# Performance work log

Hardware: AMD Instinct MI355X
Metric: run time of the kernel (lower is better)

Reference implementation:

```python
import jax, jax.numpy as jnp
import numpy as np

B, T, D_HID, D_TRK, N_TRANS = 128, 40, 512, 256, 64


def setup_inputs() -> dict:
    key = jax.random.key(0)
    ks = jax.random.split(key, 8)
    d, t = D_HID, D_TRK
    s = 0.05
    return {
        "buffers": jax.random.normal(ks[0], (B, T, 2 * d), jnp.float32),
        "W_left": jax.random.normal(ks[1], (5 * d, d), jnp.float32) * s,
        "b_left": jnp.zeros((5 * d,), jnp.float32),
        "W_right": jax.random.normal(ks[2], (5 * d, d), jnp.float32) * s,
        "W_track": jax.random.normal(ks[3], (5 * d, t), jnp.float32) * s,
        "W_ih": jax.random.normal(ks[4], (4 * t, 3 * d), jnp.float32) * s,
        "W_hh": jax.random.normal(ks[5], (4 * t, t), jnp.float32) * s,
        "b_ih": jnp.zeros((4 * t,), jnp.float32),
        "b_hh": jnp.zeros((4 * t,), jnp.float32),
        "W_trans": jax.random.normal(ks[6], (4, t), jnp.float32) * s,
        "b_trans": jnp.zeros((4,), jnp.float32),
        "transitions": jax.random.randint(ks[7], (N_TRANS, B), 0, 4),
    }


def _spinn_forward(buffers, W_left, b_left, W_right, W_track,
                   W_ih, W_hh, b_ih, b_hh, W_trans, b_trans, n_steps):
    # Thin-stack style vectorized SPINN: fixed-capacity stack + pointers.
    Bb, Tt, two_d = buffers.shape
    d = two_d // 2
    t = W_hh.shape[1]
    cap = Tt + 2  # stack never exceeds 2 initial + (T-2) shifts
    dtype = buffers.dtype

    stack0 = jnp.zeros((Bb, cap, two_d), dtype)
    # stacks = [buf[0], buf[0]] in the torch code
    stack0 = stack0.at[:, 0].set(buffers[:, 0]).at[:, 1].set(buffers[:, 0])
    sptr0 = jnp.full((Bb,), 2, jnp.int32)   # stack length
    blen0 = jnp.full((Bb,), Tt, jnp.int32)  # buffer length (pops from the end)
    th0 = jnp.zeros((Bb, t), dtype)
    tc0 = jnp.zeros((Bb, t), dtype)
    bidx = jnp.arange(Bb)

    def step(carry, _):
        stack, sptr, blen, th, tc = carry
        buf_top = buffers[bidx, blen - 1]          # buf[-1], [B, 2d]
        s1 = stack[bidx, sptr - 1]                 # stack[-1]
        s2 = stack[bidx, sptr - 2]                 # stack[-2]
        # Tracker LSTMCell on cat(buf_h, stack1_h, stack2_h)
        x = jnp.concatenate([buf_top[:, :d], s1[:, :d], s2[:, :d]], axis=1)
        gates = x @ W_ih.T + b_ih + th @ W_hh.T + b_hh
        gi, gf, gg, go = jnp.split(gates, 4, axis=1)
        tc_new = jax.nn.sigmoid(gf) * tc + jax.nn.sigmoid(gi) * jnp.tanh(gg)
        th_new = jax.nn.sigmoid(go) * jnp.tanh(tc_new)
        logits = th_new @ W_trans.T + b_trans      # [B, 4]
        trans = jnp.argmax(logits, axis=1)
        do_shift = (trans == 3) & (blen > 2)
        do_red = (trans == 2) & (sptr > 3)
        # REDUCE (TreeLSTM) computed for all rows, masked in below.
        # left = stack[-2], right = stack[-1] (right popped first in torch).
        lstm_in = (s2[:, :d] @ W_left.T + b_left
                   + s1[:, :d] @ W_right.T
                   + th_new @ W_track.T)           # [B, 5d]
        a, i_, f1, f2, o_ = jnp.split(lstm_in, 5, axis=1)
        c = (jnp.tanh(a) * jax.nn.sigmoid(i_)
             + jax.nn.sigmoid(f1) * s2[:, d:]
             + jax.nn.sigmoid(f2) * s1[:, d:])
        h = jax.nn.sigmoid(o_) * jnp.tanh(c)
        node = jnp.concatenate([h, c], axis=1)
        # SHIFT: push buf_top; REDUCE: overwrite stack[-2] and shrink by 1.
        stack = stack.at[bidx, sptr].set(
            jnp.where(do_shift[:, None], buf_top, stack[bidx, sptr]))
        stack = stack.at[bidx, sptr - 2].set(
            jnp.where(do_red[:, None], node, stack[bidx, sptr - 2]))
        sptr = sptr + do_shift.astype(jnp.int32) - do_red.astype(jnp.int32)
        blen = blen - do_shift.astype(jnp.int32)
        return (stack, sptr, blen, th_new, tc_new), logits

    _, all_logits = jax.lax.scan(step, (stack0, sptr0, blen0, th0, tc0),
                                 None, length=n_steps)
    return all_logits  # [n_steps, B, 4] = stacked trans_preds_batch


def reference(buffers, W_left, b_left, W_right, W_track, W_ih, W_hh,
              b_ih, b_hh, W_trans, b_trans, transitions):
    n_steps = transitions.shape[0]  # torch only uses transitions.size(0)
    return _spinn_forward(buffers, W_left, b_left, W_right, W_track,
                          W_ih, W_hh, b_ih, b_hh, W_trans, b_trans, n_steps)
```

## Files before the change

kernel.cpp:

```cpp
#include <hip/hip_runtime.h>
#include <math.h>


#define B_ 128
#define CAP 42
#define XW 2048
#define GSPLIT 14
#define LSPLIT 8

__device__ __forceinline__ float sigm(float x) { return 1.f / (1.f + expf(-x)); }

__global__ void k_repack(const float* __restrict__ W_ih, const float* __restrict__ W_hh,
                         const float* __restrict__ W_left, const float* __restrict__ W_right,
                         const float* __restrict__ W_track, const float* __restrict__ b_ih,
                         const float* __restrict__ b_hh,
                         float* __restrict__ W1T, float* __restrict__ W2T,
                         float* __restrict__ W3T, float* __restrict__ b1) {
    size_t idx = (size_t)blockIdx.x * 256 + threadIdx.x;
    const size_t n1 = 1792ull * 1024ull;
    const size_t n2 = 1024ull * 2560ull;
    const size_t n3 = 256ull * 2560ull;
    if (idx < n1) {
        int k = (int)(idx >> 10), n = (int)(idx & 1023);
        W1T[idx] = (k < 1536) ? W_ih[(size_t)n * 1536 + k] : W_hh[(size_t)n * 256 + (k - 1536)];
    } else if (idx < n1 + n2) {
        size_t r = idx - n1;
        int k = (int)(r / 2560), n = (int)(r % 2560);
        W2T[r] = (k < 512) ? W_right[(size_t)n * 512 + k] : W_left[(size_t)n * 512 + (k - 512)];
    } else if (idx < n1 + n2 + n3) {
        size_t r = idx - n1 - n2;
        int k = (int)(r / 2560), n = (int)(r % 2560);
        W3T[r] = W_track[(size_t)n * 256 + k];
    } else if (idx < n1 + n2 + n3 + 1024) {
        int i = (int)(idx - n1 - n2 - n3);
        b1[i] = b_ih[i] + b_hh[i];
    }
}

__global__ void k_init(const float* __restrict__ buffers, float* __restrict__ stack,
                       float* __restrict__ X, float* __restrict__ tc,
                       int* __restrict__ sptr, int* __restrict__ blen) {
    int b = blockIdx.x, t = threadIdx.x;
    const float* b0 = buffers + (size_t)b * 40 * 1024;
    const float* btop = b0 + 39 * 1024;
    float* stk = stack + (size_t)b * CAP * 1024;
    for (int j = t; j < 1024; j += 256) { stk[j] = b0[j]; stk[1024 + j] = b0[j]; }
    float* Xb = X + (size_t)b * XW;
    for (int j = t; j < 512; j += 256) {
        Xb[j] = btop[j]; Xb[512 + j] = b0[j]; Xb[1024 + j] = b0[j];
    }
    Xb[1536 + t] = 0.f;
    tc[b * 256 + t] = 0.f;
    if (t == 0) { sptr[b] = 2; blen[b] = 40; }
}

__global__ __launch_bounds__(256, 3) void k_gemm(const float* __restrict__ X,
                                                 const float* __restrict__ W1T,
                                                 const float* __restrict__ W2T,
                                                 float* __restrict__ gpart,
                                                 float* __restrict__ lpart) {
    __shared__ float As[32][132];
    __shared__ float Ws[32][68];
    const int bid = blockIdx.x;
    const float* WT; float* out; int N, n0, k0, aoff;
    if (bid < 224) {
        int ks = bid >> 4, nb = bid & 15;
        WT = W1T; out = gpart + (size_t)ks * 128 * 1024;
        N = 1024; n0 = nb * 64; k0 = ks * 128; aoff = 0;
    } else {
        int b2 = bid - 224; int ks = b2 / 40, nb = b2 % 40;
        WT = W2T; out = lpart + (size_t)ks * 128 * 2560;
        N = 2560; n0 = nb * 64; k0 = ks * 128; aoff = 512;
    }
    const int tid = threadIdx.x;
    const int tm = tid >> 4;
    const int tn = tid & 15;

    float acc[8][4];
#pragma unroll
    for (int i = 0; i < 8; i++)
#pragma unroll
        for (int j = 0; j < 4; j++) acc[i][j] = 0.f;

    for (int ki = 0; ki < 128; ki += 32) {
        const int kb = k0 + ki;
        __syncthreads();
        {
            int m = tid >> 1;
            int c8 = (tid & 1) * 16;
            const float4* src = (const float4*)(X + (size_t)m * XW + aoff + kb + c8);
#pragma unroll
            for (int j = 0; j < 4; j++) {
                float4 v = src[j];
                int kk = c8 + j * 4;
                As[kk + 0][m] = v.x; As[kk + 1][m] = v.y; As[kk + 2][m] = v.z; As[kk + 3][m] = v.w;
            }
        }
        {
            int kk = tid >> 3;
            int c = (tid & 7) * 8;
            const float4* src = (const float4*)(WT + (size_t)(kb + kk) * N + n0 + c);
            float4* dst = (float4*)(&Ws[kk][c]);
            dst[0] = src[0]; dst[1] = src[1];
        }
        __syncthreads();
#pragma unroll 4
        for (int kk = 0; kk < 32; kk++) {
            float a[8], w[4];
            *(float4*)&a[0] = *(const float4*)&As[kk][tm * 4];
            *(float4*)&a[4] = *(const float4*)&As[kk][64 + tm * 4];
            *(float4*)&w[0] = *(const float4*)&Ws[kk][tn * 4];
#pragma unroll
            for (int i = 0; i < 8; i++)
#pragma unroll
                for (int j = 0; j < 4; j++) acc[i][j] += a[i] * w[j];
        }
    }
    float* base = out + n0 + tn * 4;
#pragma unroll
    for (int i = 0; i < 8; i++) {
        int m = (i < 4) ? (tm * 4 + i) : (64 + tm * 4 + (i - 4));
        *(float4*)(base + (size_t)m * N) = make_float4(acc[i][0], acc[i][1], acc[i][2], acc[i][3]);
    }
}

__global__ __launch_bounds__(256) void k_B(const float* __restrict__ gpart,
                                           const float* __restrict__ lpart,
                                           const float* __restrict__ b1,
                                           const float* __restrict__ b_left,
                                           const float* __restrict__ W3T,
                                           const float* __restrict__ W_trans,
                                           const float* __restrict__ b_trans,
                                           const float* __restrict__ buffers,
                                           float* __restrict__ stack,
                                           float* __restrict__ X,
                                           const float* __restrict__ tc_in,
                                           float* __restrict__ tc_out,
                                           const int* __restrict__ sp_in,
                                           int* __restrict__ sp_out,
                                           const int* __restrict__ bl_in,
                                           int* __restrict__ bl_out,
                                           float* __restrict__ out_s) {
    const int bid = blockIdx.x;
    const int b = bid >> 2, q = bid & 3;
    const int t = threadIdx.x;
    const int sp = sp_in[b], bl = bl_in[b];

    const float* gp = gpart + (size_t)b * 1024;
    float gi = b1[t], gf = b1[256 + t], gg = b1[512 + t], go = b1[768 + t];
#pragma unroll
    for (int kc = 0; kc < GSPLIT; kc++) {
        const float* p = gp + (size_t)kc * 128 * 1024;
        gi += p[t]; gf += p[256 + t]; gg += p[512 + t]; go += p[768 + t];
    }
    float tcv = tc_in[b * 256 + t];
    float tcn = sigm(gf) * tcv + sigm(gi) * tanhf(gg);
    float thn = sigm(go) * tanhf(tcn);

    __shared__ float sh_th[256];
    __shared__ float red[256][4];
    sh_th[t] = thn;
    red[t][0] = thn * W_trans[t];
    red[t][1] = thn * W_trans[256 + t];
    red[t][2] = thn * W_trans[512 + t];
    red[t][3] = thn * W_trans[768 + t];
    __syncthreads();
    for (int off = 128; off > 0; off >>= 1) {
        if (t < off) {
            red[t][0] += red[t + off][0]; red[t][1] += red[t + off][1];
            red[t][2] += red[t + off][2]; red[t][3] += red[t + off][3];
        }
        __syncthreads();
    }
    float lg[4]; int tr = 0; float best = -1e30f;
#pragma unroll
    for (int l = 0; l < 4; l++) {
        lg[l] = red[0][l] + b_trans[l];
        if (lg[l] > best) { best = lg[l]; tr = l; }
    }
    if (q == 0 && t == 0) {
#pragma unroll
        for (int l = 0; l < 4; l++) out_s[b * 4 + l] = lg[l];
    }
    const bool do_shift = (tr == 3) && (bl > 2);
    const bool do_red   = (tr == 2) && (sp > 3);
    const int spn = sp + (do_shift ? 1 : 0) - (do_red ? 1 : 0);
    const int bln = bl - (do_shift ? 1 : 0);
    float* stk = stack + (size_t)b * CAP * 1024;

    float node_h = 0.f;
    if (do_red && t < 128) {
        const int j = q * 128 + t;
        const float* lp = lpart + (size_t)b * 2560;
        float a  = b_left[j],        ii = b_left[512 + j], f1 = b_left[1024 + j],
              f2 = b_left[1536 + j], oo = b_left[2048 + j];
#pragma unroll
        for (int kc = 0; kc < LSPLIT; kc++) {
            const float* p = lp + (size_t)kc * 128 * 2560;
            a += p[j]; ii += p[512 + j]; f1 += p[1024 + j]; f2 += p[1536 + j]; oo += p[2048 + j];
        }
        const float* w = W3T + j;
#pragma unroll 4
        for (int k = 0; k < 256; k++) {
            float th = sh_th[k];
            const float* wk = w + (size_t)k * 2560;
            a += th * wk[0]; ii += th * wk[512]; f1 += th * wk[1024];
            f2 += th * wk[1536]; oo += th * wk[2048];
        }
        float s1c = stk[(size_t)(sp - 1) * 1024 + 512 + j];
        float s2c = stk[(size_t)(sp - 2) * 1024 + 512 + j];
        float c = tanhf(a) * sigm(ii) + sigm(f1) * s2c + sigm(f2) * s1c;
        float h = sigm(oo) * tanhf(c);
        stk[(size_t)(sp - 2) * 1024 + j] = h;
        stk[(size_t)(sp - 2) * 1024 + 512 + j] = c;
        node_h = h;
    }
    if (do_shift) {
        const float* bt = buffers + ((size_t)b * 40 + (bl - 1)) * 1024;
        const int idx = q * 256 + t;
        stk[(size_t)sp * 1024 + idx] = bt[idx];
    }
    float* Xb = X + (size_t)b * XW;
    if (t < 128) {
        const int j = q * 128 + t;
        const float* btn = buffers + ((size_t)b * 40 + (bln - 1)) * 1024;
        Xb[j] = btn[j];
        float s1h;
        if (do_red)        s1h = node_h;
        else if (do_shift) s1h = buffers[((size_t)b * 40 + (bl - 1)) * 1024 + j];
        else               s1h = stk[(size_t)(sp - 1) * 1024 + j];
        Xb[512 + j] = s1h;
        Xb[1024 + j] = stk[(size_t)(spn - 2) * 1024 + j];
    }
    if ((t >> 6) == q) {
        Xb[1536 + t] = thn;
        tc_out[b * 256 + t] = tcn;
    }
    if (q == 0 && t == 0) { sp_out[b] = spn; bl_out[b] = bln; }
}

extern "C" void kernel_launch(void* const* d_in, const int* in_sizes, int n_in,
                              void* d_out, int out_size, void* d_ws, size_t ws_size,
                              hipStream_t stream) {
    const float* buffers = (const float*)d_in[0];
    const float* W_left  = (const float*)d_in[1];
    const float* b_left  = (const float*)d_in[2];
    const float* W_right = (const float*)d_in[3];
    const float* W_track = (const float*)d_in[4];
    const float* W_ih    = (const float*)d_in[5];
    const float* W_hh    = (const float*)d_in[6];
    const float* b_ih    = (const float*)d_in[7];
    const float* b_hh    = (const float*)d_in[8];
    const float* W_trans = (const float*)d_in[9];
    const float* b_trans = (const float*)d_in[10];
    float* out = (float*)d_out;

    float* ws = (float*)d_ws;
    size_t off = 0;
    float* W1T   = ws + off; off += 1792ull * 1024;
    float* W2T   = ws + off; off += 1024ull * 2560;
    float* W3T   = ws + off; off += 256ull * 2560;
    float* b1    = ws + off; off += 1024;
    float* X     = ws + off; off += (size_t)B_ * XW;
    float* tc_a  = ws + off; off += (size_t)B_ * 256;
    float* tc_b  = ws + off; off += (size_t)B_ * 256;
    float* gpart = ws + off; off += (size_t)GSPLIT * B_ * 1024;
    float* lpart = ws + off; off += (size_t)LSPLIT * B_ * 2560;
    float* stack = ws + off; off += (size_t)B_ * CAP * 1024;
    int* sp_a = (int*)(ws + off); off += 128;
    int* sp_b = (int*)(ws + off); off += 128;
    int* bl_a = (int*)(ws + off); off += 128;
    int* bl_b = (int*)(ws + off); off += 128;

    {
        size_t total = 1792ull * 1024 + 1024ull * 2560 + 256ull * 2560 + 1024;
        int blocks = (int)((total + 255) / 256);
        k_repack<<<blocks, 256, 0, stream>>>(W_ih, W_hh, W_left, W_right, W_track, b_ih, b_hh,
                                             W1T, W2T, W3T, b1);
        k_init<<<B_, 256, 0, stream>>>(buffers, stack, X, tc_a, sp_a, bl_a);
    }

    for (int s = 0; s < 64; s++) {
        k_gemm<<<544, 256, 0, stream>>>(X, W1T, W2T, gpart, lpart);
        const float* tci = (s & 1) ? tc_b : tc_a;  float* tco = (s & 1) ? tc_a : tc_b;
        const int*   spi = (s & 1) ? sp_b : sp_a;  int*   spo = (s & 1) ? sp_a : sp_b;
        const int*   bli = (s & 1) ? bl_b : bl_a;  int*   blo = (s & 1) ? bl_a : bl_b;
        k_B<<<512, 256, 0, stream>>>(gpart, lpart, b1, b_left, W3T, W_trans, b_trans,
                                     buffers, stack, X, tci, tco, spi, spo, bli, blo,
                                     out + (size_t)s * B_ * 4);
    }
    (void)in_sizes; (void)n_in; (void)out_size; (void)ws_size;
}
```

Baseline: 2.547 ms.

## Use 128x128 GEMM tiles with deeper split-K, wave-shuffle reduce, split W3T loop

Adds a GEMM mode that uses 128-wide output tiles with 8x8 per-thread accumulators and half the K-chunk per block, doubling the split-K partial count. Blocks therefore get higher arithmetic intensity while the grid stays at 544 blocks. The mode is chosen at runtime from workspace size, and k_B now sums a variable number of partials. k_B's logit reduction moves from a shared-memory tree to wavefront shuffles, and the reduce-path W3T dot product is split across both thread halves and combined through shared memory. Stack capacity and the X row width are trimmed. In exchange, k_B reads twice as many partial sums from memory and the GEMM kernel holds more registers per thread.

```diff
diff --git a/kernel.cpp b/kernel.cpp
--- a/kernel.cpp
+++ b/kernel.cpp
@@ -3,10 +3,9 @@
 
 
 #define B_ 128
-#define CAP 42
-#define XW 2048
-#define GSPLIT 14
-#define LSPLIT 8
+#define CAP 40
+#define XW 1792
+#define NSTEP 64
 
 __device__ __forceinline__ float sigm(float x) { return 1.f / (1.f + expf(-x)); }
 
@@ -58,69 +57,124 @@
                                                  const float* __restrict__ W1T,
                                                  const float* __restrict__ W2T,
                                                  float* __restrict__ gpart,
-                                                 float* __restrict__ lpart) {
+                                                 float* __restrict__ lpart, int mode) {
     __shared__ float As[32][132];
-    __shared__ float Ws[32][68];
+    __shared__ float Ws[32][132];
     const int bid = blockIdx.x;
-    const float* WT; float* out; int N, n0, k0, aoff;
-    if (bid < 224) {
-        int ks = bid >> 4, nb = bid & 15;
-        WT = W1T; out = gpart + (size_t)ks * 128 * 1024;
-        N = 1024; n0 = nb * 64; k0 = ks * 128; aoff = 0;
+    const int tid = threadIdx.x;
+    const int tm = tid >> 4, tn = tid & 15;
+
+    if (mode) {
+        const float* WT; float* out; int N, n0, k0, aoff;
+        if (bid < 224) {
+            int ks = bid >> 3, nb = bid & 7;
+            WT = W1T; out = gpart + (size_t)ks * 131072;
+            N = 1024; n0 = nb * 128; k0 = ks * 64; aoff = 0;
+        } else {
+            int tI = bid - 224; int ks = tI / 20, nb = tI % 20;
+            WT = W2T; out = lpart + (size_t)ks * 327680;
+            N = 2560; n0 = nb * 128; k0 = ks * 64; aoff = 512;
+        }
+        float acc[8][8];
+#pragma unroll
+        for (int i = 0; i < 8; i++)
+#pragma unroll
+            for (int j = 0; j < 8; j++) acc[i][j] = 0.f;
+
+        for (int ki = 0; ki < 64; ki += 32) {
+            const int kb = k0 + ki;
+            __syncthreads();
+            {
+                int m = tid >> 1, c8 = (tid & 1) * 16;
+                const float4* src = (const float4*)(X + (size_t)m * XW + aoff + kb + c8);
+#pragma unroll
+                for (int j = 0; j < 4; j++) {
+                    float4 v = src[j];
+                    int kk = c8 + j * 4;
+                    As[kk + 0][m] = v.x; As[kk + 1][m] = v.y; As[kk + 2][m] = v.z; As[kk + 3][m] = v.w;
+                }
+            }
+            {
+                int kk = tid >> 3, c = (tid & 7) * 16;
+                const float4* src = (const float4*)(WT + (size_t)(kb + kk) * N + n0 + c);
+                float4* dst = (float4*)(&Ws[kk][c]);
+                dst[0] = src[0]; dst[1] = src[1]; dst[2] = src[2]; dst[3] = src[3];
+            }
+            __syncthreads();
+#pragma unroll 4
+            for (int kk = 0; kk < 32; kk++) {
+                float a[8], w[8];
+                *(float4*)&a[0] = *(const float4*)&As[kk][tm * 4];
+                *(float4*)&a[4] = *(const float4*)&As[kk][64 + tm * 4];
+                *(float4*)&w[0] = *(const float4*)&Ws[kk][tn * 4];
+                *(float4*)&w[4] = *(const float4*)&Ws[kk][64 + tn * 4];
+#pragma unroll
+                for (int i = 0; i < 8; i++)
+#pragma unroll
+                    for (int j = 0; j < 8; j++) acc[i][j] += a[i] * w[j];
+            }
+        }
+        float* base = out + n0;
+#pragma unroll
+        for (int i = 0; i < 8; i++) {
+            int m = (i < 4) ? (tm * 4 + i) : (64 + tm * 4 + (i - 4));
+            float* p = base + (size_t)m * N;
+            *(float4*)(p + tn * 4) = make_float4(acc[i][0], acc[i][1], acc[i][2], acc[i][3]);
+            *(float4*)(p + 64 + tn * 4) = make_float4(acc[i][4], acc[i][5], acc[i][6], acc[i][7]);
+        }
     } else {
-        int b2 = bid - 224; int ks = b2 / 40, nb = b2 % 40;
-        WT = W2T; out = lpart + (size_t)ks * 128 * 2560;
-        N = 2560; n0 = nb * 64; k0 = ks * 128; aoff = 512;
-    }
-    const int tid = threadIdx.x;
-    const int tm = tid >> 4;
-    const int tn = tid & 15;
-
-    float acc[8][4];
-#pragma unroll
-    for (int i = 0; i < 8; i++)
-#pragma unroll
-        for (int j = 0; j < 4; j++) acc[i][j] = 0.f;
-
-    for (int ki = 0; ki < 128; ki += 32) {
-        const int kb = k0 + ki;
-        __syncthreads();
-        {
-            int m = tid >> 1;
-            int c8 = (tid & 1) * 16;
-            const float4* src = (const float4*)(X + (size_t)m * XW + aoff + kb + c8);
-#pragma unroll
-            for (int j = 0; j < 4; j++) {
-                float4 v = src[j];
-                int kk = c8 + j * 4;
-                As[kk + 0][m] = v.x; As[kk + 1][m] = v.y; As[kk + 2][m] = v.z; As[kk + 3][m] = v.w;
-            }
-        }
-        {
-            int kk = tid >> 3;
-            int c = (tid & 7) * 8;
-            const float4* src = (const float4*)(WT + (size_t)(kb + kk) * N + n0 + c);
-            float4* dst = (float4*)(&Ws[kk][c]);
-            dst[0] = src[0]; dst[1] = src[1];
-        }
-        __syncthreads();
+        const float* WT; float* out; int N, n0, k0, aoff;
+        if (bid < 224) {
+            int ks = bid >> 4, nb = bid & 15;
+            WT = W1T; out = gpart + (size_t)ks * 131072;
+            N = 1024; n0 = nb * 64; k0 = ks * 128; aoff = 0;
+        } else {
+            int tI = bid - 224; int ks = tI / 40, nb = tI % 40;
+            WT = W2T; out = lpart + (size_t)ks * 327680;
+            N = 2560; n0 = nb * 64; k0 = ks * 128; aoff = 512;
+        }
+        float acc[8][4];
+#pragma unroll
+        for (int i = 0; i < 8; i++)
+#pragma unroll
+            for (int j = 0; j < 4; j++) acc[i][j] = 0.f;
+
+        for (int ki = 0; ki < 128; ki += 32) {
+            const int kb = k0 + ki;
+            __syncthreads();
+            {   int m = tid >> 1, c8 = (tid & 1) * 16;
+                const float4* src = (const float4*)(X + (size_t)m * XW + aoff + kb + c8);
+#pragma unroll
+                for (int j = 0; j < 4; j++) {
+                    float4 v = src[j];
+                    int kk = c8 + j * 4;
+                    As[kk + 0][m] = v.x; As[kk + 1][m] = v.y; As[kk + 2][m] = v.z; As[kk + 3][m] = v.w;
+                }
+            }
+            {   int kk = tid >> 3, c = (tid & 7) * 8;
+                const float4* src = (const float4*)(WT + (size_t)(kb + kk) * N + n0 + c);
+                float4* dst = (float4*)(&Ws[kk][c]);
+                dst[0] = src[0]; dst[1] = src[1];
+            }
+            __syncthreads();
 #pragma unroll 4
-        for (int kk = 0; kk < 32; kk++) {
-            float a[8], w[4];
-            *(float4*)&a[0] = *(const float4*)&As[kk][tm * 4];
-            *(float4*)&a[4] = *(const float4*)&As[kk][64 + tm * 4];
-            *(float4*)&w[0] = *(const float4*)&Ws[kk][tn * 4];
-#pragma unroll
-            for (int i = 0; i < 8; i++)
-#pragma unroll
-                for (int j = 0; j < 4; j++) acc[i][j] += a[i] * w[j];
-        }
-    }
-    float* base = out + n0 + tn * 4;
-#pragma unroll
-    for (int i = 0; i < 8; i++) {
-        int m = (i < 4) ? (tm * 4 + i) : (64 + tm * 4 + (i - 4));
-        *(float4*)(base + (size_t)m * N) = make_float4(acc[i][0], acc[i][1], acc[i][2], acc[i][3]);
+            for (int kk = 0; kk < 32; kk++) {
+                float a[8], w[4];
+                *(float4*)&a[0] = *(const float4*)&As[kk][tm * 4];
+                *(float4*)&a[4] = *(const float4*)&As[kk][64 + tm * 4];
+                *(float4*)&w[0] = *(const float4*)&Ws[kk][tn * 4];
+#pragma unroll
+                for (int i = 0; i < 8; i++)
+#pragma unroll
+                    for (int j = 0; j < 4; j++) acc[i][j] += a[i] * w[j];
+            }
+        }
+        float* base = out + n0 + tn * 4;
+#pragma unroll
+        for (int i = 0; i < 8; i++) {
+            int m = (i < 4) ? (tm * 4 + i) : (64 + tm * 4 + (i - 4));
+            *(float4*)(base + (size_t)m * N) = make_float4(acc[i][0], acc[i][1], acc[i][2], acc[i][3]);
+        }
     }
 }
 
@@ -140,73 +194,90 @@
                                            int* __restrict__ sp_out,
                                            const int* __restrict__ bl_in,
                                            int* __restrict__ bl_out,
-                                           float* __restrict__ out_s) {
+                                           float* __restrict__ out_s,
+                                           int gsplit, int lsplit) {
     const int bid = blockIdx.x;
     const int b = bid >> 2, q = bid & 3;
     const int t = threadIdx.x;
     const int sp = sp_in[b], bl = bl_in[b];
+    __shared__ float sh_th[256];
+    __shared__ float redw[4][4];
+    __shared__ float shg[5][128];
 
     const float* gp = gpart + (size_t)b * 1024;
     float gi = b1[t], gf = b1[256 + t], gg = b1[512 + t], go = b1[768 + t];
-#pragma unroll
-    for (int kc = 0; kc < GSPLIT; kc++) {
-        const float* p = gp + (size_t)kc * 128 * 1024;
+#pragma unroll 4
+    for (int kc = 0; kc < gsplit; kc++) {
+        const float* p = gp + (size_t)kc * 131072;
         gi += p[t]; gf += p[256 + t]; gg += p[512 + t]; go += p[768 + t];
     }
     float tcv = tc_in[b * 256 + t];
     float tcn = sigm(gf) * tcv + sigm(gi) * tanhf(gg);
     float thn = sigm(go) * tanhf(tcn);
-
-    __shared__ float sh_th[256];
-    __shared__ float red[256][4];
+    if ((t >> 6) == q) tc_out[b * 256 + t] = tcn;
     sh_th[t] = thn;
-    red[t][0] = thn * W_trans[t];
-    red[t][1] = thn * W_trans[256 + t];
-    red[t][2] = thn * W_trans[512 + t];
-    red[t][3] = thn * W_trans[768 + t];
+
+    float v0 = thn * W_trans[t],       v1 = thn * W_trans[256 + t];
+    float v2 = thn * W_trans[512 + t], v3 = thn * W_trans[768 + t];
+#pragma unroll
+    for (int off = 32; off > 0; off >>= 1) {
+        v0 += __shfl_down(v0, off); v1 += __shfl_down(v1, off);
+        v2 += __shfl_down(v2, off); v3 += __shfl_down(v3, off);
+    }
+    if ((t & 63) == 0) {
+        int w = t >> 6;
+        redw[w][0] = v0; redw[w][1] = v1; redw[w][2] = v2; redw[w][3] = v3;
+    }
     __syncthreads();
-    for (int off = 128; off > 0; off >>= 1) {
-        if (t < off) {
-            red[t][0] += red[t + off][0]; red[t][1] += red[t + off][1];
-            red[t][2] += red[t + off][2]; red[t][3] += red[t + off][3];
-        }
-        __syncthreads();
-    }
-    float lg[4]; int tr = 0; float best = -1e30f;
-#pragma unroll
-    for (int l = 0; l < 4; l++) {
-        lg[l] = red[0][l] + b_trans[l];
-        if (lg[l] > best) { best = lg[l]; tr = l; }
-    }
-    if (q == 0 && t == 0) {
-#pragma unroll
-        for (int l = 0; l < 4; l++) out_s[b * 4 + l] = lg[l];
-    }
+    float lg0 = redw[0][0] + redw[1][0] + redw[2][0] + redw[3][0] + b_trans[0];
+    float lg1 = redw[0][1] + redw[1][1] + redw[2][1] + redw[3][1] + b_trans[1];
+    float lg2 = redw[0][2] + redw[1][2] + redw[2][2] + redw[3][2] + b_trans[2];
+    float lg3 = redw[0][3] + redw[1][3] + redw[2][3] + redw[3][3] + b_trans[3];
+    int tr = 0; float best = lg0;
+    if (lg1 > best) { best = lg1; tr = 1; }
+    if (lg2 > best) { best = lg2; tr = 2; }
+    if (lg3 > best) { best = lg3; tr = 3; }
     const bool do_shift = (tr == 3) && (bl > 2);
     const bool do_red   = (tr == 2) && (sp > 3);
     const int spn = sp + (do_shift ? 1 : 0) - (do_red ? 1 : 0);
     const int bln = bl - (do_shift ? 1 : 0);
+    if (q == 0 && t == 0) {
+        out_s[b * 4 + 0] = lg0; out_s[b * 4 + 1] = lg1;
+        out_s[b * 4 + 2] = lg2; out_s[b * 4 + 3] = lg3;
+        sp_out[b] = spn; bl_out[b] = bln;
+    }
     float* stk = stack + (size_t)b * CAP * 1024;
 
+    const int jj = t & 127, kh = t >> 7, j = q * 128 + jj;
     float node_h = 0.f;
-    if (do_red && t < 128) {
-        const int j = q * 128 + t;
+    float a, ii, f1, f2, oo;
+    if (do_red) {
+        if (kh == 0) {
+            a  = b_left[j];        ii = b_left[512 + j]; f1 = b_left[1024 + j];
+            f2 = b_left[1536 + j]; oo = b_left[2048 + j];
+        } else { a = ii = f1 = f2 = oo = 0.f; }
         const float* lp = lpart + (size_t)b * 2560;
-        float a  = b_left[j],        ii = b_left[512 + j], f1 = b_left[1024 + j],
-              f2 = b_left[1536 + j], oo = b_left[2048 + j];
-#pragma unroll
-        for (int kc = 0; kc < LSPLIT; kc++) {
-            const float* p = lp + (size_t)kc * 128 * 2560;
+        const int half = lsplit >> 1;
+        for (int kc = kh * half; kc < kh * half + half; kc++) {
+            const float* p = lp + (size_t)kc * 327680;
             a += p[j]; ii += p[512 + j]; f1 += p[1024 + j]; f2 += p[1536 + j]; oo += p[2048 + j];
         }
         const float* w = W3T + j;
 #pragma unroll 4
-        for (int k = 0; k < 256; k++) {
+        for (int k = kh * 128; k < kh * 128 + 128; k++) {
             float th = sh_th[k];
             const float* wk = w + (size_t)k * 2560;
             a += th * wk[0]; ii += th * wk[512]; f1 += th * wk[1024];
             f2 += th * wk[1536]; oo += th * wk[2048];
         }
+        if (kh == 1) {
+            shg[0][jj] = a; shg[1][jj] = ii; shg[2][jj] = f1; shg[3][jj] = f2; shg[4][jj] = oo;
+        }
+    }
+    __syncthreads();
+    if (do_red && kh == 0) {
+        a += shg[0][jj]; ii += shg[1][jj]; f1 += shg[2][jj];
+        f2 += shg[3][jj]; oo += shg[4][jj];
         float s1c = stk[(size_t)(sp - 1) * 1024 + 512 + j];
         float s2c = stk[(size_t)(sp - 2) * 1024 + 512 + j];
         float c = tanhf(a) * sigm(ii) + sigm(f1) * s2c + sigm(f2) * s1c;
@@ -221,8 +292,7 @@
         stk[(size_t)sp * 1024 + idx] = bt[idx];
     }
     float* Xb = X + (size_t)b * XW;
-    if (t < 128) {
-        const int j = q * 128 + t;
+    if (kh == 0) {
         const float* btn = buffers + ((size_t)b * 40 + (bln - 1)) * 1024;
         Xb[j] = btn[j];
         float s1h;
@@ -232,11 +302,7 @@
         Xb[512 + j] = s1h;
         Xb[1024 + j] = stk[(size_t)(spn - 2) * 1024 + j];
     }
-    if ((t >> 6) == q) {
-        Xb[1536 + t] = thn;
-        tc_out[b * 256 + t] = tcn;
-    }
-    if (q == 0 && t == 0) { sp_out[b] = spn; bl_out[b] = bln; }
+    if ((t >> 6) == q) Xb[1536 + t] = thn;
 }
 
 extern "C" void kernel_launch(void* const* d_in, const int* in_sizes, int n_in,
@@ -257,15 +323,22 @@
 
     float* ws = (float*)d_ws;
     size_t off = 0;
-    float* W1T   = ws + off; off += 1792ull * 1024;
-    float* W2T   = ws + off; off += 1024ull * 2560;
-    float* W3T   = ws + off; off += 256ull * 2560;
-    float* b1    = ws + off; off += 1024;
-    float* X     = ws + off; off += (size_t)B_ * XW;
-    float* tc_a  = ws + off; off += (size_t)B_ * 256;
-    float* tc_b  = ws + off; off += (size_t)B_ * 256;
-    float* gpart = ws + off; off += (size_t)GSPLIT * B_ * 1024;
-    float* lpart = ws + off; off += (size_t)LSPLIT * B_ * 2560;
+    float* W1T  = ws + off; off += 1792ull * 1024;
+    float* W2T  = ws + off; off += 1024ull * 2560;
+    float* W3T  = ws + off; off += 256ull * 2560;
+    float* b1   = ws + off; off += 1024;
+    float* X    = ws + off; off += (size_t)B_ * XW;
+    float* tc_a = ws + off; off += (size_t)B_ * 256;
+    float* tc_b = ws + off; off += (size_t)B_ * 256;
+
+    size_t needA = (off + 28ull * 131072 + 16ull * 327680
+                    + (size_t)B_ * CAP * 1024 + 512) * sizeof(float);
+    const int mode   = (ws_size >= needA) ? 1 : 0;
+    const int gsplit = mode ? 28 : 14;
+    const int lsplit = mode ? 16 : 8;
+
+    float* gpart = ws + off; off += (size_t)gsplit * 131072;
+    float* lpart = ws + off; off += (size_t)lsplit * 327680;
     float* stack = ws + off; off += (size_t)B_ * CAP * 1024;
     int* sp_a = (int*)(ws + off); off += 128;
     int* sp_b = (int*)(ws + off); off += 128;
@@ -280,14 +353,14 @@
         k_init<<<B_, 256, 0, stream>>>(buffers, stack, X, tc_a, sp_a, bl_a);
     }
 
-    for (int s = 0; s < 64; s++) {
-        k_gemm<<<544, 256, 0, stream>>>(X, W1T, W2T, gpart, lpart);
+    for (int s = 0; s < NSTEP; s++) {
+        k_gemm<<<544, 256, 0, stream>>>(X, W1T, W2T, gpart, lpart, mode);
         const float* tci = (s & 1) ? tc_b : tc_a;  float* tco = (s & 1) ? tc_a : tc_b;
         const int*   spi = (s & 1) ? sp_b : sp_a;  int*   spo = (s & 1) ? sp_a : sp_b;
         const int*   bli = (s & 1) ? bl_b : bl_a;  int*   blo = (s & 1) ? bl_a : bl_b;
         k_B<<<512, 256, 0, stream>>>(gpart, lpart, b1, b_left, W3T, W_trans, b_trans,
                                      buffers, stack, X, tci, tco, spi, spo, bli, blo,
-                                     out + (size_t)s * B_ * 4);
+                                     out + (size_t)s * B_ * 4, gsplit, lsplit);
     }
     (void)in_sizes; (void)n_in; (void)out_size; (void)ws_size;
 }
```

Result: slower. 2.803 ms (+10.1%).

## Move recurrent W_hh product into per-step cell kernel and split reduce-path work

Applied to the files above, without the earlier changes.

The tracker's h@W_hh contribution is no longer part of the big per-step GEMM. Each k_B block now computes it for the next step from the new hidden state in shared memory, using a separately transposed WhhT, and stores it in a double-buffered hh array. This drops the GEMM's K split from 14 to 12 and its grid from 544 to 512 blocks. The logit reduction switches from a shared-memory tree to wave shuffles, and the REDUCE path splits its K loop across both halves of the block. In exchange, every k_B block now does a 256x256 matvec slice with strided global loads, and the stack capacity shrinks to 40, which may be tight.

```diff
diff --git a/kernel.cpp b/kernel.cpp
--- a/kernel.cpp
+++ b/kernel.cpp
@@ -3,10 +3,11 @@
 
 
 #define B_ 128
-#define CAP 42
-#define XW 2048
-#define GSPLIT 14
+#define CAP 40
+#define XW 1536
+#define GSPLIT 12
 #define LSPLIT 8
+#define NSTEP 64
 
 __device__ __forceinline__ float sigm(float x) { return 1.f / (1.f + expf(-x)); }
 
@@ -15,14 +16,16 @@
                          const float* __restrict__ W_track, const float* __restrict__ b_ih,
                          const float* __restrict__ b_hh,
                          float* __restrict__ W1T, float* __restrict__ W2T,
-                         float* __restrict__ W3T, float* __restrict__ b1) {
+                         float* __restrict__ W3T, float* __restrict__ WhhT,
+                         float* __restrict__ b1) {
     size_t idx = (size_t)blockIdx.x * 256 + threadIdx.x;
-    const size_t n1 = 1792ull * 1024ull;
+    const size_t n1 = 1536ull * 1024ull;
     const size_t n2 = 1024ull * 2560ull;
     const size_t n3 = 256ull * 2560ull;
+    const size_t n4 = 256ull * 1024ull;
     if (idx < n1) {
         int k = (int)(idx >> 10), n = (int)(idx & 1023);
-        W1T[idx] = (k < 1536) ? W_ih[(size_t)n * 1536 + k] : W_hh[(size_t)n * 256 + (k - 1536)];
+        W1T[idx] = W_ih[(size_t)n * 1536 + k];
     } else if (idx < n1 + n2) {
         size_t r = idx - n1;
         int k = (int)(r / 2560), n = (int)(r % 2560);
@@ -31,14 +34,19 @@
         size_t r = idx - n1 - n2;
         int k = (int)(r / 2560), n = (int)(r % 2560);
         W3T[r] = W_track[(size_t)n * 256 + k];
-    } else if (idx < n1 + n2 + n3 + 1024) {
-        int i = (int)(idx - n1 - n2 - n3);
+    } else if (idx < n1 + n2 + n3 + n4) {
+        size_t r = idx - n1 - n2 - n3;
+        int k = (int)(r >> 10), n = (int)(r & 1023);
+        WhhT[r] = W_hh[(size_t)n * 256 + k];
+    } else if (idx < n1 + n2 + n3 + n4 + 1024) {
+        int i = (int)(idx - n1 - n2 - n3 - n4);
         b1[i] = b_ih[i] + b_hh[i];
     }
 }
 
 __global__ void k_init(const float* __restrict__ buffers, float* __restrict__ stack,
                        float* __restrict__ X, float* __restrict__ tc,
+                       float* __restrict__ hh,
                        int* __restrict__ sptr, int* __restrict__ blen) {
     int b = blockIdx.x, t = threadIdx.x;
     const float* b0 = buffers + (size_t)b * 40 * 1024;
@@ -49,8 +57,8 @@
     for (int j = t; j < 512; j += 256) {
         Xb[j] = btop[j]; Xb[512 + j] = b0[j]; Xb[1024 + j] = b0[j];
     }
-    Xb[1536 + t] = 0.f;
     tc[b * 256 + t] = 0.f;
+    for (int j = t; j < 1024; j += 256) hh[(size_t)b * 1024 + j] = 0.f;
     if (t == 0) { sptr[b] = 2; blen[b] = 40; }
 }
 
@@ -63,13 +71,13 @@
     __shared__ float Ws[32][68];
     const int bid = blockIdx.x;
     const float* WT; float* out; int N, n0, k0, aoff;
-    if (bid < 224) {
+    if (bid < 192) {
         int ks = bid >> 4, nb = bid & 15;
-        WT = W1T; out = gpart + (size_t)ks * 128 * 1024;
+        WT = W1T; out = gpart + (size_t)ks * 131072;
         N = 1024; n0 = nb * 64; k0 = ks * 128; aoff = 0;
     } else {
-        int b2 = bid - 224; int ks = b2 / 40, nb = b2 % 40;
-        WT = W2T; out = lpart + (size_t)ks * 128 * 2560;
+        int tI = bid - 192; int ks = tI / 40, nb = tI % 40;
+        WT = W2T; out = lpart + (size_t)ks * 327680;
         N = 2560; n0 = nb * 64; k0 = ks * 128; aoff = 512;
     }
     const int tid = threadIdx.x;
@@ -126,9 +134,12 @@
 
 __global__ __launch_bounds__(256) void k_B(const float* __restrict__ gpart,
                                            const float* __restrict__ lpart,
+                                           const float* __restrict__ hh_in,
+                                           float* __restrict__ hh_out,
                                            const float* __restrict__ b1,
                                            const float* __restrict__ b_left,
                                            const float* __restrict__ W3T,
+                                           const float* __restrict__ WhhT,
                                            const float* __restrict__ W_trans,
                                            const float* __restrict__ b_trans,
                                            const float* __restrict__ buffers,
@@ -145,68 +156,99 @@
     const int b = bid >> 2, q = bid & 3;
     const int t = threadIdx.x;
     const int sp = sp_in[b], bl = bl_in[b];
+    __shared__ float sh_th[256];
+    __shared__ float redw[4][4];
+    __shared__ float shg[5][128];
 
     const float* gp = gpart + (size_t)b * 1024;
-    float gi = b1[t], gf = b1[256 + t], gg = b1[512 + t], go = b1[768 + t];
-#pragma unroll
+    const float* hp = hh_in + (size_t)b * 1024;
+    float gi = b1[t] + hp[t],             gf = b1[256 + t] + hp[256 + t];
+    float gg = b1[512 + t] + hp[512 + t], go = b1[768 + t] + hp[768 + t];
+#pragma unroll 4
     for (int kc = 0; kc < GSPLIT; kc++) {
-        const float* p = gp + (size_t)kc * 128 * 1024;
+        const float* p = gp + (size_t)kc * 131072;
         gi += p[t]; gf += p[256 + t]; gg += p[512 + t]; go += p[768 + t];
     }
     float tcv = tc_in[b * 256 + t];
     float tcn = sigm(gf) * tcv + sigm(gi) * tanhf(gg);
     float thn = sigm(go) * tanhf(tcn);
-
-    __shared__ float sh_th[256];
-    __shared__ float red[256][4];
+    if ((t >> 6) == q) tc_out[b * 256 + t] = tcn;
     sh_th[t] = thn;
-    red[t][0] = thn * W_trans[t];
-    red[t][1] = thn * W_trans[256 + t];
-    red[t][2] = thn * W_trans[512 + t];
-    red[t][3] = thn * W_trans[768 + t];
+
+    float v0 = thn * W_trans[t],       v1 = thn * W_trans[256 + t];
+    float v2 = thn * W_trans[512 + t], v3 = thn * W_trans[768 + t];
+#pragma unroll
+    for (int off = 32; off > 0; off >>= 1) {
+        v0 += __shfl_down(v0, off); v1 += __shfl_down(v1, off);
+        v2 += __shfl_down(v2, off); v3 += __shfl_down(v3, off);
+    }
+    if ((t & 63) == 0) {
+        int w = t >> 6;
+        redw[w][0] = v0; redw[w][1] = v1; redw[w][2] = v2; redw[w][3] = v3;
+    }
     __syncthreads();
-    for (int off = 128; off > 0; off >>= 1) {
-        if (t < off) {
-            red[t][0] += red[t + off][0]; red[t][1] += red[t + off][1];
-            red[t][2] += red[t + off][2]; red[t][3] += red[t + off][3];
-        }
-        __syncthreads();
-    }
-    float lg[4]; int tr = 0; float best = -1e30f;
-#pragma unroll
-    for (int l = 0; l < 4; l++) {
-        lg[l] = red[0][l] + b_trans[l];
-        if (lg[l] > best) { best = lg[l]; tr = l; }
-    }
-    if (q == 0 && t == 0) {
-#pragma unroll
-        for (int l = 0; l < 4; l++) out_s[b * 4 + l] = lg[l];
-    }
+    float lg0 = redw[0][0] + redw[1][0] + redw[2][0] + redw[3][0] + b_trans[0];
+    float lg1 = redw[0][1] + redw[1][1] + redw[2][1] + redw[3][1] + b_trans[1];
+    float lg2 = redw[0][2] + redw[1][2] + redw[2][2] + redw[3][2] + b_trans[2];
+    float lg3 = redw[0][3] + redw[1][3] + redw[2][3] + redw[3][3] + b_trans[3];
+    int tr = 0; float best = lg0;
+    if (lg1 > best) { best = lg1; tr = 1; }
+    if (lg2 > best) { best = lg2; tr = 2; }
+    if (lg3 > best) { best = lg3; tr = 3; }
     const bool do_shift = (tr == 3) && (bl > 2);
     const bool do_red   = (tr == 2) && (sp > 3);
     const int spn = sp + (do_shift ? 1 : 0) - (do_red ? 1 : 0);
     const int bln = bl - (do_shift ? 1 : 0);
+    if (q == 0 && t == 0) {
+        out_s[b * 4 + 0] = lg0; out_s[b * 4 + 1] = lg1;
+        out_s[b * 4 + 2] = lg2; out_s[b * 4 + 3] = lg3;
+        sp_out[b] = spn; bl_out[b] = bln;
+    }
     float* stk = stack + (size_t)b * CAP * 1024;
 
+    {
+        const float* wh = WhhT + q * 256 + t;
+        float h0 = 0, h1 = 0, h2 = 0, h3 = 0;
+#pragma unroll 8
+        for (int k = 0; k < 256; k += 4) {
+            h0 += sh_th[k]     * wh[(size_t)k * 1024];
+            h1 += sh_th[k + 1] * wh[(size_t)(k + 1) * 1024];
+            h2 += sh_th[k + 2] * wh[(size_t)(k + 2) * 1024];
+            h3 += sh_th[k + 3] * wh[(size_t)(k + 3) * 1024];
+        }
+        hh_out[(size_t)b * 1024 + q * 256 + t] = (h0 + h1) + (h2 + h3);
+    }
+
+    const int jj = t & 127, kh = t >> 7, j = q * 128 + jj;
     float node_h = 0.f;
-    if (do_red && t < 128) {
-        const int j = q * 128 + t;
+    float a, ii, f1, f2, oo;
+    if (do_red) {
+        if (kh == 0) {
+            a  = b_left[j];        ii = b_left[512 + j]; f1 = b_left[1024 + j];
+            f2 = b_left[1536 + j]; oo = b_left[2048 + j];
+        } else { a = ii = f1 = f2 = oo = 0.f; }
         const float* lp = lpart + (size_t)b * 2560;
-        float a  = b_left[j],        ii = b_left[512 + j], f1 = b_left[1024 + j],
-              f2 = b_left[1536 + j], oo = b_left[2048 + j];
-#pragma unroll
-        for (int kc = 0; kc < LSPLIT; kc++) {
-            const float* p = lp + (size_t)kc * 128 * 2560;
+        const int half = LSPLIT >> 1;
+        for (int kc = kh * half; kc < kh * half + half; kc++) {
+            const float* p = lp + (size_t)kc * 327680;
             a += p[j]; ii += p[512 + j]; f1 += p[1024 + j]; f2 += p[1536 + j]; oo += p[2048 + j];
         }
         const float* w = W3T + j;
 #pragma unroll 4
-        for (int k = 0; k < 256; k++) {
+        for (int k = kh * 128; k < kh * 128 + 128; k++) {
             float th = sh_th[k];
             const float* wk = w + (size_t)k * 2560;
             a += th * wk[0]; ii += th * wk[512]; f1 += th * wk[1024];
             f2 += th * wk[1536]; oo += th * wk[2048];
         }
+        if (kh == 1) {
+            shg[0][jj] = a; shg[1][jj] = ii; shg[2][jj] = f1; shg[3][jj] = f2; shg[4][jj] = oo;
+        }
+    }
+    __syncthreads();
+    if (do_red && kh == 0) {
+        a += shg[0][jj]; ii += shg[1][jj]; f1 += shg[2][jj];
+        f2 += shg[3][jj]; oo += shg[4][jj];
         float s1c = stk[(size_t)(sp - 1) * 1024 + 512 + j];
         float s2c = stk[(size_t)(sp - 2) * 1024 + 512 + j];
         float c = tanhf(a) * sigm(ii) + sigm(f1) * s2c + sigm(f2) * s1c;
@@ -221,8 +263,7 @@
         stk[(size_t)sp * 1024 + idx] = bt[idx];
     }
     float* Xb = X + (size_t)b * XW;
-    if (t < 128) {
-        const int j = q * 128 + t;
+    if (kh == 0) {
         const float* btn = buffers + ((size_t)b * 40 + (bln - 1)) * 1024;
         Xb[j] = btn[j];
         float s1h;
@@ -232,11 +273,6 @@
         Xb[512 + j] = s1h;
         Xb[1024 + j] = stk[(size_t)(spn - 2) * 1024 + j];
     }
-    if ((t >> 6) == q) {
-        Xb[1536 + t] = thn;
-        tc_out[b * 256 + t] = tcn;
-    }
-    if (q == 0 && t == 0) { sp_out[b] = spn; bl_out[b] = bln; }
 }
 
 extern "C" void kernel_launch(void* const* d_in, const int* in_sizes, int n_in,
@@ -257,15 +293,18 @@
 
     float* ws = (float*)d_ws;
     size_t off = 0;
-    float* W1T   = ws + off; off += 1792ull * 1024;
+    float* W1T   = ws + off; off += 1536ull * 1024;
     float* W2T   = ws + off; off += 1024ull * 2560;
     float* W3T   = ws + off; off += 256ull * 2560;
+    float* WhhT  = ws + off; off += 256ull * 1024;
     float* b1    = ws + off; off += 1024;
     float* X     = ws + off; off += (size_t)B_ * XW;
     float* tc_a  = ws + off; off += (size_t)B_ * 256;
     float* tc_b  = ws + off; off += (size_t)B_ * 256;
-    float* gpart = ws + off; off += (size_t)GSPLIT * B_ * 1024;
-    float* lpart = ws + off; off += (size_t)LSPLIT * B_ * 2560;
+    float* hh_a  = ws + off; off += (size_t)B_ * 1024;
+    float* hh_b  = ws + off; off += (size_t)B_ * 1024;
+    float* gpart = ws + off; off += (size_t)GSPLIT * 131072;
+    float* lpart = ws + off; off += (size_t)LSPLIT * 327680;
     float* stack = ws + off; off += (size_t)B_ * CAP * 1024;
     int* sp_a = (int*)(ws + off); off += 128;
     int* sp_b = (int*)(ws + off); off += 128;
@@ -273,21 +312,22 @@
     int* bl_b = (int*)(ws + off); off += 128;
 
     {
-        size_t total = 1792ull * 1024 + 1024ull * 2560 + 256ull * 2560 + 1024;
+        size_t total = 1536ull * 1024 + 1024ull * 2560 + 256ull * 2560 + 256ull * 1024 + 1024;
         int blocks = (int)((total + 255) / 256);
         k_repack<<<blocks, 256, 0, stream>>>(W_ih, W_hh, W_left, W_right, W_track, b_ih, b_hh,
-                                             W1T, W2T, W3T, b1);
-        k_init<<<B_, 256, 0, stream>>>(buffers, stack, X, tc_a, sp_a, bl_a);
-    }
-
-    for (int s = 0; s < 64; s++) {
-        k_gemm<<<544, 256, 0, stream>>>(X, W1T, W2T, gpart, lpart);
+                                             W1T, W2T, W3T, WhhT, b1);
+        k_init<<<B_, 256, 0, stream>>>(buffers, stack, X, tc_a, hh_a, sp_a, bl_a);
+    }
+
+    for (int s = 0; s < NSTEP; s++) {
+        k_gemm<<<512, 256, 0, stream>>>(X, W1T, W2T, gpart, lpart);
         const float* tci = (s & 1) ? tc_b : tc_a;  float* tco = (s & 1) ? tc_a : tc_b;
+        const float* hhi = (s & 1) ? hh_b : hh_a;  float* hho = (s & 1) ? hh_a : hh_b;
         const int*   spi = (s & 1) ? sp_b : sp_a;  int*   spo = (s & 1) ? sp_a : sp_b;
         const int*   bli = (s & 1) ? bl_b : bl_a;  int*   blo = (s & 1) ? bl_a : bl_b;
-        k_B<<<512, 256, 0, stream>>>(gpart, lpart, b1, b_left, W3T, W_trans, b_trans,
-                                     buffers, stack, X, tci, tco, spi, spo, bli, blo,
-                                     out + (size_t)s * B_ * 4);
+        k_B<<<512, 256, 0, stream>>>(gpart, lpart, hhi, hho, b1, b_left, W3T, WhhT,
+                                     W_trans, b_trans, buffers, stack, X, tci, tco,
+                                     spi, spo, bli, blo, out + (size_t)s * B_ * 4);
     }
     (void)in_sizes; (void)n_in; (void)out_size; (void)ws_size;
 }
```

New measurement: 2.472 ms. 1.03x faster.
